# Kernel tuning notes

Measured on AMD Instinct MI355X. Metric: run time of the kernel, lower is better.

The kernel has to match this reference:

```python
import jax, jax.numpy as jnp
import numpy as np

N_MAP, N_ACT, B, E_PER, D = 131072, 1024, 16, 16384, 128
MAP_PER, ACT_PER = N_MAP // B, N_ACT // B
E = B * E_PER
EPS = 1e-5  # torch GroupNorm default eps


def _gn(x, g, b):
    # GroupNorm(1, C) on [N, C]: per-row normalization over channels
    m = jnp.mean(x, -1, keepdims=True)
    v = jnp.mean((x - m) ** 2, -1, keepdims=True)
    return (x - m) * jax.lax.rsqrt(v + EPS) * g + b


def _lin_gn(x, W, g, b, act=True):
    # LaneGCN Linear: nn.Linear(bias=False) -> GroupNorm(1, n_out) -> optional ReLU
    y = _gn(x @ W.T, g, b)
    return jax.nn.relu(y) if act else y


def setup_inputs() -> dict:
    key = jax.random.key(0)
    keys = iter(jax.random.split(key, 64))
    nrm = lambda shape, s=1.0: jax.random.normal(next(keys), shape, jnp.float32) * s
    uni = lambda shape, s=1.0: jax.random.uniform(next(keys), shape, jnp.float32) * s
    inp = {}
    inp['feat'] = nrm((N_MAP, D))
    inp['turn'] = nrm((N_MAP, 2))
    inp['control'] = uni((N_MAP,))
    inp['intersect'] = uni((N_MAP,))
    inp['map_ctrs'] = uni((N_MAP, 2), 100.0)
    inp['actors'] = nrm((N_ACT, D))
    inp['actor_ctrs'] = uni((N_ACT, 2), 100.0)
    # fixed within-scene edge list (stands in for the distance-threshold nonzero)
    rng = np.random.default_rng(0)
    hi = np.concatenate([rng.integers(b * MAP_PER, (b + 1) * MAP_PER, E_PER) for b in range(B)])
    wi = np.concatenate([rng.integers(b * ACT_PER, (b + 1) * ACT_PER, E_PER) for b in range(B)])
    inp['hi'] = jnp.asarray(hi, jnp.int32)
    inp['wi'] = jnp.asarray(wi, jnp.int32)
    # parameters
    W = lambda *s: nrm(s, 0.02)
    g_ = lambda *s: 1.0 + nrm(s, 0.05)
    b_ = lambda *s: nrm(s, 0.05)
    inp['meta_W'], inp['meta_g'], inp['meta_b'] = W(D, D + 4), g_(D), b_(D)
    inp['dW1'], inp['db1'] = W(2, D, 2), b_(2, D)
    inp['dW2'], inp['dg2'], inp['dbt2'] = W(2, D, D), g_(2, D), b_(2, D)
    inp['qW'], inp['qg'], inp['qb'] = W(2, D, D), g_(2, D), b_(2, D)
    inp['cW1'], inp['cg1'], inp['cb1'] = W(2, D, 3 * D), g_(2, D), b_(2, D)
    inp['cW2'] = W(2, D, D)
    inp['aW'] = W(2, D, D)
    inp['ng_g'], inp['ng_b'] = g_(2, D), b_(2, D)
    inp['lW'], inp['lg'], inp['lb'] = W(2, D, D), g_(2, D), b_(2, D)
    return inp


def reference(feat, turn, control, intersect, map_ctrs, actors, actor_ctrs, hi, wi,
              meta_W, meta_g, meta_b, dW1, db1, dW2, dg2, dbt2, qW, qg, qb,
              cW1, cg1, cb1, cW2, aW, ng_g, ng_b, lW, lg, lb):
    # meta fuse: concat(feat, turn, control, intersect) -> Linear+GN+ReLU
    meta = jnp.concatenate([feat, turn, control[:, None], intersect[:, None]], axis=1)
    feat = _lin_gn(meta, meta_W, meta_g, meta_b)
    for i in range(2):  # two Att blocks
        res = feat
        # dist branch: raw ctr offsets -> Linear(2,n_ctx)+ReLU -> Linear+GN+ReLU
        d = map_ctrs[hi] - actor_ctrs[wi]                       # [E, 2]
        d = jax.nn.relu(d @ dW1[i].T + db1[i])                  # [E, D]
        d = _lin_gn(d, dW2[i], dg2[i], dbt2[i])
        q = _lin_gn(feat[hi], qW[i], qg[i], qb[i])              # query on gathered agts
        c = jnp.concatenate([d, q, actors[wi]], axis=1)         # [E, 3D]
        c = _lin_gn(c, cW1[i], cg1[i], cb1[i])
        c = c @ cW2[i].T                                        # bias-free Linear
        a = feat @ aW[i].T                                      # self path, bias-free
        a = a.at[hi].add(c)                                     # scatter-add messages
        a = jax.nn.relu(_gn(a, ng_g[i], ng_b[i]))
        a = _lin_gn(a, lW[i], lg[i], lb[i], act=False)
        feat = jax.nn.relu(a + res)                             # use_relu=True
    return feat
```

## Files before the change

kernel.cpp:

```cpp
#include <hip/hip_runtime.h>
#include <stdint.h>

typedef unsigned short u16;
typedef __bf16 bf16x8 __attribute__((ext_vector_type(8)));
typedef float f32x4 __attribute__((ext_vector_type(4)));

#define MFMA(a, b, c) __builtin_amdgcn_mfma_f32_16x16x32_bf16(a, b, c, 0, 0, 0)

__device__ __forceinline__ u16 f2bf(float f) {
    union { float f; unsigned u; } v; v.f = f;
    unsigned r = v.u + 0x7fffu + ((v.u >> 16) & 1u);
    return (u16)(r >> 16);
}
__device__ __forceinline__ float bf2f(u16 h) {
    union { unsigned u; float f; } v; v.u = ((unsigned)h) << 16; return v.f;
}
__device__ __forceinline__ bf16x8 as_frag(uint4 u) {
    union { uint4 u; bf16x8 b; } v; v.u = u; return v.b;
}
__device__ __forceinline__ bf16x8 ldg_frag(const u16* p) {
    return as_frag(*reinterpret_cast<const uint4*>(p));
}
__device__ __forceinline__ int rowmap(int t, int i) {
    return 32 * (t >> 1) + 8 * (i >> 2) + 4 * (t & 1) + (i & 3);
}

template <int SRC_LDU>
__device__ __forceinline__ void stage128(const u16* __restrict__ src, u16* dst, int tid, int nt) {
    for (int c = tid; c < 2048; c += nt) {
        int row = c >> 4, j = c & 15;
        int js = (j & 8) | ((j ^ row) & 7);
        *reinterpret_cast<uint4*>(dst + row * 128 + js * 8) =
            *reinterpret_cast<const uint4*>(src + row * SRC_LDU + j * 8);
    }
}
__device__ __forceinline__ bf16x8 lds_w(const u16* base, int row, int byteoff) {
    int off = row * 256 + (byteoff ^ ((row & 7) << 4));
    return as_frag(*reinterpret_cast<const uint4*>(reinterpret_cast<const char*>(base) + off));
}

template <int KT>
__device__ __forceinline__ void gemm_acc(const bf16x8* a, const u16* __restrict__ W, int ldw,
                                         f32x4* acc, int c16, int q4) {
#pragma unroll
    for (int n = 0; n < 8; n++) {
        const u16* wp = W + (size_t)(n * 16 + c16) * ldw + q4 * 8;
#pragma unroll
        for (int k = 0; k < KT; k++) {
            bf16x8 b = ldg_frag(wp + k * 32);
            acc[n] = MFMA(a[k], b, acc[n]);
        }
    }
}

__device__ __forceinline__ void gn_t(f32x4* acc, const float* __restrict__ gb, bool relu, int q4) {
    float s = 0.f, s2 = 0.f;
#pragma unroll
    for (int t = 0; t < 8; t++)
#pragma unroll
        for (int r = 0; r < 4; r++) { float x = acc[t][r]; s += x; s2 = fmaf(x, x, s2); }
    s += __shfl_xor(s, 16, 64); s += __shfl_xor(s, 32, 64);
    s2 += __shfl_xor(s2, 16, 64); s2 += __shfl_xor(s2, 32, 64);
    float mean = s * (1.f / 128.f);
    float var = fmaf(s2, 1.f / 128.f, -mean * mean);
    float rstd = rsqrtf(var + 1e-5f);
#pragma unroll
    for (int t = 0; t < 8; t++) {
        const float4* g4 = reinterpret_cast<const float4*>(gb + (t * 16 + q4 * 4) * 2);
        float4 p01 = g4[0], p23 = g4[1];
        float gv[4] = {p01.x, p01.z, p23.x, p23.z};
        float bv[4] = {p01.y, p01.w, p23.y, p23.w};
#pragma unroll
        for (int r = 0; r < 4; r++) {
            float y = fmaf((acc[t][r] - mean) * rstd, gv[r], bv[r]);
            acc[t][r] = relu ? fmaxf(y, 0.f) : y;
        }
    }
}

__device__ __forceinline__ bf16x8 pack_frag(f32x4 lo, f32x4 hi) {
    union { u16 s[8]; bf16x8 b; } t;
#pragma unroll
    for (int j = 0; j < 4; j++) { t.s[j] = f2bf(lo[j]); t.s[4 + j] = f2bf(hi[j]); }
    return t.b;
}

__device__ __forceinline__ void gn_c(f32x4* acc, const float* __restrict__ g,
                                     const float* __restrict__ b, bool relu, int c16) {
    float gs[8], bs[8];
#pragma unroll
    for (int n = 0; n < 8; n++) { gs[n] = g[n * 16 + c16]; bs[n] = b[n * 16 + c16]; }
#pragma unroll
    for (int r = 0; r < 4; r++) {
        float s = 0.f, s2 = 0.f;
#pragma unroll
        for (int n = 0; n < 8; n++) { float x = acc[n][r]; s += x; s2 = fmaf(x, x, s2); }
#pragma unroll
        for (int m = 1; m < 16; m <<= 1) { s += __shfl_xor(s, m, 64); s2 += __shfl_xor(s2, m, 64); }
        float mean = s * (1.f / 128.f);
        float var = fmaf(s2, 1.f / 128.f, -mean * mean);
        float rstd = rsqrtf(var + 1e-5f);
#pragma unroll
        for (int n = 0; n < 8; n++) {
            float y = fmaf((acc[n][r] - mean) * rstd, gs[n], bs[n]);
            acc[n][r] = relu ? fmaxf(y, 0.f) : y;
        }
    }
}

__global__ __launch_bounds__(256) void k_prep(
    const float* __restrict__ dW2s, const float* __restrict__ qWs, const float* __restrict__ cW1s,
    const float* __restrict__ cW2s, const float* __restrict__ aWs, const float* __restrict__ lWs,
    const float* __restrict__ actors, const float* __restrict__ metaW,
    const float* __restrict__ dW1s, const float* __restrict__ db1s,
    const float* __restrict__ dg2s, const float* __restrict__ dbt2s,
    const float* __restrict__ qgs, const float* __restrict__ qbs,
    const float* __restrict__ cg1s, const float* __restrict__ cb1s,
    u16* __restrict__ o_dW2p, u16* __restrict__ o_qW, u16* __restrict__ o_cW1p,
    u16* __restrict__ o_cW2, u16* __restrict__ o_aW, u16* __restrict__ o_lW,
    u16* __restrict__ o_actb, u16* __restrict__ o_mWf, float* __restrict__ o_mWe,
    float* __restrict__ o_dw1p, float* __restrict__ o_gb) {
    int idx = blockIdx.x * 256 + threadIdx.x;
    if (idx >= 412672) return;
    if (idx < 32768) {
        int i = idx >> 14, rem = idx & 16383, ro = rem >> 7, col = rem & 127;
        o_dW2p[idx] = f2bf(dW2s[i * 16384 + rowmap(ro >> 4, ro & 15) * 128 + col]);
    } else if (idx < 65536) {
        int j = idx - 32768; o_qW[j] = f2bf(qWs[j]);
    } else if (idx < 163840) {
        int j = idx - 65536, i = j / 49152, rem = j - i * 49152, ro = rem / 384, col = rem - ro * 384;
        o_cW1p[j] = f2bf(cW1s[i * 49152 + rowmap(ro >> 4, ro & 15) * 384 + col]);
    } else if (idx < 196608) { int j = idx - 163840; o_cW2[j] = f2bf(cW2s[j]); }
    else if (idx < 229376) { int j = idx - 196608; o_aW[j] = f2bf(aWs[j]); }
    else if (idx < 262144) { int j = idx - 229376; o_lW[j] = f2bf(lWs[j]); }
    else if (idx < 393216) { int j = idx - 262144; o_actb[j] = f2bf(actors[j]); }
    else if (idx < 409600) { int j = idx - 393216; o_mWf[j] = f2bf(metaW[(j >> 7) * 132 + (j & 127)]); }
    else if (idx < 410112) { int j = idx - 409600; o_mWe[j] = metaW[(j >> 2) * 132 + 128 + (j & 3)]; }
    else if (idx < 411136) {
        int j = idx - 410112, i = j >> 9, col = (j >> 2) & 127, t = j & 3;
        float v = (t == 0) ? dW1s[i * 256 + col * 2]
                : (t == 1) ? dW1s[i * 256 + col * 2 + 1]
                : (t == 2) ? db1s[i * 128 + col] : 0.f;
        o_dw1p[j] = v;
    } else {
        int j = idx - 411136;
        int tb = j >> 9, rem = j & 511, i = rem >> 8, q = rem & 255, o = q >> 1, f = q & 1;
        const float* gsrc = (tb == 0) ? dg2s : (tb == 1) ? qgs : cg1s;
        const float* bsrc = (tb == 0) ? dbt2s : (tb == 1) ? qbs : cb1s;
        int src = i * 128 + rowmap(o >> 4, o & 15);
        o_gb[j] = f ? bsrc[src] : gsrc[src];
    }
}

__global__ __launch_bounds__(256) void k_meta(
    const float* __restrict__ feat, const float* __restrict__ turn,
    const float* __restrict__ ctrl, const float* __restrict__ inter,
    const u16* __restrict__ mWf, const float* __restrict__ mWe,
    const float* __restrict__ g, const float* __restrict__ b, u16* __restrict__ out) {
    int lane = threadIdx.x & 63, wv = threadIdx.x >> 6;
    int c16 = lane & 15, q4 = lane >> 4;
    int m0 = (blockIdx.x * 4 + wv) * 16;
    bf16x8 a[4];
    const float* xr = feat + (size_t)(m0 + c16) * 128 + q4 * 8;
#pragma unroll
    for (int k = 0; k < 4; k++) {
        float4 u0 = *reinterpret_cast<const float4*>(xr + k * 32);
        float4 u1 = *reinterpret_cast<const float4*>(xr + k * 32 + 4);
        union { u16 s[8]; bf16x8 b; } t;
        t.s[0] = f2bf(u0.x); t.s[1] = f2bf(u0.y); t.s[2] = f2bf(u0.z); t.s[3] = f2bf(u0.w);
        t.s[4] = f2bf(u1.x); t.s[5] = f2bf(u1.y); t.s[6] = f2bf(u1.z); t.s[7] = f2bf(u1.w);
        a[k] = t.b;
    }
    f32x4 acc[8] = {};
    gemm_acc<4>(a, mWf, 128, acc, c16, q4);
#pragma unroll
    for (int r = 0; r < 4; r++) {
        int row = m0 + q4 * 4 + r;
        float t0 = turn[2 * row], t1 = turn[2 * row + 1];
        float cv = ctrl[row], iv = inter[row];
#pragma unroll
        for (int n = 0; n < 8; n++) {
            int col = n * 16 + c16;
            float4 we = reinterpret_cast<const float4*>(mWe)[col];
            acc[n][r] += t0 * we.x + t1 * we.y + cv * we.z + iv * we.w;
        }
    }
    gn_c(acc, g, b, true, c16);
#pragma unroll
    for (int r = 0; r < 4; r++) {
        size_t row = m0 + q4 * 4 + r;
#pragma unroll
        for (int n = 0; n < 8; n++) out[row * 128 + n * 16 + c16] = f2bf(acc[n][r]);
    }
}

__global__ __launch_bounds__(256) void k_nodeA(
    const u16* __restrict__ featb, const u16* __restrict__ qW, const u16* __restrict__ aW,
    const float* __restrict__ qg, const float* __restrict__ qb,
    u16* __restrict__ q_out, float* __restrict__ a_out) {
    int lane = threadIdx.x & 63, wv = threadIdx.x >> 6;
    int c16 = lane & 15, q4 = lane >> 4;
    int m0 = (blockIdx.x * 4 + wv) * 16;
    bf16x8 a[4];
    const u16* xr = featb + (size_t)(m0 + c16) * 128 + q4 * 8;
#pragma unroll
    for (int k = 0; k < 4; k++) a[k] = ldg_frag(xr + k * 32);
    f32x4 accq[8] = {}, acca[8] = {};
    gemm_acc<4>(a, qW, 128, accq, c16, q4);
    gemm_acc<4>(a, aW, 128, acca, c16, q4);
#pragma unroll
    for (int r = 0; r < 4; r++) {
        size_t row = m0 + q4 * 4 + r;
#pragma unroll
        for (int n = 0; n < 8; n++) a_out[row * 128 + n * 16 + c16] = acca[n][r];
    }
    gn_c(accq, qg, qb, true, c16);
#pragma unroll
    for (int r = 0; r < 4; r++) {
        size_t row = m0 + q4 * 4 + r;
#pragma unroll
        for (int n = 0; n < 8; n++) q_out[row * 128 + n * 16 + c16] = f2bf(accq[n][r]);
    }
}

__global__ __launch_bounds__(256) void k_edge(
    const int* __restrict__ hi, const int* __restrict__ wi,
    const float* __restrict__ mctr, const float* __restrict__ actr,
    const float* __restrict__ dw1p, const u16* __restrict__ dW2p,
    const float* __restrict__ gb_d2,
    const u16* __restrict__ q_node, const u16* __restrict__ actb,
    const u16* __restrict__ cW1p, const float* __restrict__ gb_c1,
    const u16* __restrict__ cW2, float* __restrict__ a_out) {
    __shared__ u16 s0[16384];
    __shared__ u16 s1[16384];
    int tid = threadIdx.x;
    int lane = tid & 63, wv = tid >> 6;
    int c16 = lane & 15, q4 = lane >> 4;
    int bid = (int)blockIdx.x;
    bid = (bid & 7) * 256 + (bid >> 3);
    int ebase = bid * 128 + wv * 32;
    int h0 = hi[ebase + c16], w0 = wi[ebase + c16];
    int h1 = hi[ebase + 16 + c16], w1 = wi[ebase + 16 + c16];
    stage128<128>(dW2p, s0, tid, 256);
    stage128<384>(cW1p, s1, tid, 256);
    bf16x8 qf0[4], qf1[4], af0[4], af1[4];
    {
        const u16* qr0 = q_node + (size_t)h0 * 128 + q4 * 8;
        const u16* qr1 = q_node + (size_t)h1 * 128 + q4 * 8;
        const u16* ar0 = actb + (size_t)w0 * 128 + q4 * 8;
        const u16* ar1 = actb + (size_t)w1 * 128 + q4 * 8;
#pragma unroll
        for (int k = 0; k < 4; k++) {
            qf0[k] = ldg_frag(qr0 + k * 32); qf1[k] = ldg_frag(qr1 + k * 32);
            af0[k] = ldg_frag(ar0 + k * 32); af1[k] = ldg_frag(ar1 + k * 32);
        }
    }
    float dx0 = mctr[2 * h0] - actr[2 * w0], dy0 = mctr[2 * h0 + 1] - actr[2 * w0 + 1];
    float dx1 = mctr[2 * h1] - actr[2 * w1], dy1 = mctr[2 * h1 + 1] - actr[2 * w1 + 1];
    bf16x8 bd0[4], bd1[4];
    const float4* w4p = reinterpret_cast<const float4*>(dw1p);
#pragma unroll
    for (int k = 0; k < 4; k++) {
        union { u16 s[8]; uint4 u; } t0, t1;
#pragma unroll
        for (int j = 0; j < 8; j++) {
            float4 w4 = w4p[k * 32 + q4 * 8 + j];
            t0.s[j] = f2bf(fmaxf(fmaf(dx0, w4.x, fmaf(dy0, w4.y, w4.z)), 0.f));
            t1.s[j] = f2bf(fmaxf(fmaf(dx1, w4.x, fmaf(dy1, w4.y, w4.z)), 0.f));
        }
        bd0[k] = as_frag(t0.u); bd1[k] = as_frag(t1.u);
    }
    __syncthreads();
    f32x4 accA[8] = {}, accB[8] = {};
#pragma unroll
    for (int k = 0; k < 4; k++)
#pragma unroll
        for (int t = 0; t < 8; t++) {
            bf16x8 a = lds_w(s0, t * 16 + c16, k * 64 + q4 * 16);
            accA[t] = MFMA(a, bd0[k], accA[t]);
            accB[t] = MFMA(a, bd1[k], accB[t]);
        }
    gn_t(accA, gb_d2, true, q4);
    gn_t(accB, gb_d2, true, q4);
    bf16x8 d2f0[4], d2f1[4];
#pragma unroll
    for (int k = 0; k < 4; k++) {
        d2f0[k] = pack_frag(accA[2 * k], accA[2 * k + 1]);
        d2f1[k] = pack_frag(accB[2 * k], accB[2 * k + 1]);
    }
    f32x4 cA[8] = {}, cB[8] = {};
#pragma unroll
    for (int k = 0; k < 4; k++)
#pragma unroll
        for (int t = 0; t < 8; t++) {
            bf16x8 a = lds_w(s1, t * 16 + c16, k * 64 + q4 * 16);
            cA[t] = MFMA(a, d2f0[k], cA[t]);
            cB[t] = MFMA(a, d2f1[k], cB[t]);
        }
    __syncthreads();
    stage128<384>(cW1p + 128, s0, tid, 256);
    stage128<384>(cW1p + 256, s1, tid, 256);
    __syncthreads();
#pragma unroll
    for (int k = 0; k < 4; k++)
#pragma unroll
        for (int t = 0; t < 8; t++) {
            bf16x8 a = lds_w(s0, t * 16 + c16, k * 64 + q4 * 16);
            cA[t] = MFMA(a, qf0[k], cA[t]);
            cB[t] = MFMA(a, qf1[k], cB[t]);
        }
#pragma unroll
    for (int k = 0; k < 4; k++)
#pragma unroll
        for (int t = 0; t < 8; t++) {
            bf16x8 a = lds_w(s1, t * 16 + c16, k * 64 + q4 * 16);
            cA[t] = MFMA(a, af0[k], cA[t]);
            cB[t] = MFMA(a, af1[k], cB[t]);
        }
    __syncthreads();
    stage128<128>(cW2, s0, tid, 256);
    gn_t(cA, gb_c1, true, q4);
    gn_t(cB, gb_c1, true, q4);
    bf16x8 ba0[4], ba1[4];
#pragma unroll
    for (int k = 0; k < 4; k++) {
        ba0[k] = pack_frag(cA[2 * k], cA[2 * k + 1]);
        ba1[k] = pack_frag(cB[2 * k], cB[2 * k + 1]);
    }
    __syncthreads();
    f32x4 oA[8] = {}, oB[8] = {};
#pragma unroll
    for (int k = 0; k < 4; k++)
#pragma unroll
        for (int n = 0; n < 8; n++) {
            bf16x8 b = lds_w(s0, n * 16 + c16, k * 64 + q4 * 16);
            oA[n] = MFMA(ba0[k], b, oA[n]);
            oB[n] = MFMA(ba1[k], b, oB[n]);
        }
#pragma unroll
    for (int r = 0; r < 4; r++) {
        int hr0 = hi[ebase + q4 * 4 + r];
        int hr1 = hi[ebase + 16 + q4 * 4 + r];
        float* dst0 = a_out + (size_t)hr0 * 128 + c16;
        float* dst1 = a_out + (size_t)hr1 * 128 + c16;
#pragma unroll
        for (int n = 0; n < 8; n++) {
            unsafeAtomicAdd(dst0 + n * 16, oA[n][r]);
            unsafeAtomicAdd(dst1 + n * 16, oB[n][r]);
        }
    }
}

__global__ __launch_bounds__(256) void k_nodeB(
    const float* __restrict__ a_in, const float* __restrict__ gg, const float* __restrict__ gb,
    const u16* __restrict__ lW, const float* __restrict__ lg, const float* __restrict__ lb,
    const u16* __restrict__ res, u16* __restrict__ out_bf, float* __restrict__ out_f32) {
    int lane = threadIdx.x & 63, wv = threadIdx.x >> 6;
    int c16 = lane & 15, q4 = lane >> 4;
    int m0 = (blockIdx.x * 4 + wv) * 16;
    const float* xr = a_in + (size_t)(m0 + c16) * 128 + q4 * 8;
    float x[32];
#pragma unroll
    for (int k = 0; k < 4; k++) {
        float4 u0 = *reinterpret_cast<const float4*>(xr + k * 32);
        float4 u1 = *reinterpret_cast<const float4*>(xr + k * 32 + 4);
        x[k * 8 + 0] = u0.x; x[k * 8 + 1] = u0.y; x[k * 8 + 2] = u0.z; x[k * 8 + 3] = u0.w;
        x[k * 8 + 4] = u1.x; x[k * 8 + 5] = u1.y; x[k * 8 + 6] = u1.z; x[k * 8 + 7] = u1.w;
    }
    float s = 0.f, s2 = 0.f;
#pragma unroll
    for (int t = 0; t < 32; t++) { s += x[t]; s2 = fmaf(x[t], x[t], s2); }
    s += __shfl_xor(s, 16, 64); s += __shfl_xor(s, 32, 64);
    s2 += __shfl_xor(s2, 16, 64); s2 += __shfl_xor(s2, 32, 64);
    float mean = s * (1.f / 128.f);
    float var = fmaf(s2, 1.f / 128.f, -mean * mean);
    float rstd = rsqrtf(var + 1e-5f);
    bf16x8 a[4];
#pragma unroll
    for (int k = 0; k < 4; k++) {
        float4 g0 = *reinterpret_cast<const float4*>(gg + k * 32 + q4 * 8);
        float4 g1 = *reinterpret_cast<const float4*>(gg + k * 32 + q4 * 8 + 4);
        float4 b0 = *reinterpret_cast<const float4*>(gb + k * 32 + q4 * 8);
        float4 b1 = *reinterpret_cast<const float4*>(gb + k * 32 + q4 * 8 + 4);
        float gv[8] = {g0.x, g0.y, g0.z, g0.w, g1.x, g1.y, g1.z, g1.w};
        float bv[8] = {b0.x, b0.y, b0.z, b0.w, b1.x, b1.y, b1.z, b1.w};
        union { u16 s[8]; bf16x8 b; } t;
#pragma unroll
        for (int j = 0; j < 8; j++) {
            float y = fmaf((x[k * 8 + j] - mean) * rstd, gv[j], bv[j]);
            t.s[j] = f2bf(fmaxf(y, 0.f));
        }
        a[k] = t.b;
    }
    f32x4 acc[8] = {};
    gemm_acc<4>(a, lW, 128, acc, c16, q4);
    gn_c(acc, lg, lb, false, c16);
#pragma unroll
    for (int r = 0; r < 4; r++) {
        size_t row = m0 + q4 * 4 + r;
#pragma unroll
        for (int n = 0; n < 8; n++) {
            int col = n * 16 + c16;
            float y = acc[n][r] + bf2f(res[row * 128 + col]);
            y = fmaxf(y, 0.f);
            if (out_bf) out_bf[row * 128 + col] = f2bf(y);
            else out_f32[row * 128 + col] = y;
        }
    }
}

extern "C" void kernel_launch(void* const* d_in, const int* in_sizes, int n_in,
                              void* d_out, int out_size, void* d_ws, size_t ws_size,
                              hipStream_t stream) {
    const float* feat = (const float*)d_in[0];
    const float* turn = (const float*)d_in[1];
    const float* ctrl = (const float*)d_in[2];
    const float* inter = (const float*)d_in[3];
    const float* mctr = (const float*)d_in[4];
    const float* actors = (const float*)d_in[5];
    const float* actr = (const float*)d_in[6];
    const int* hi = (const int*)d_in[7];
    const int* wi = (const int*)d_in[8];
    const float* metaW = (const float*)d_in[9];
    const float* metag = (const float*)d_in[10];
    const float* metab = (const float*)d_in[11];
    const float* dW1 = (const float*)d_in[12];
    const float* db1 = (const float*)d_in[13];
    const float* dW2 = (const float*)d_in[14];
    const float* dg2 = (const float*)d_in[15];
    const float* dbt2 = (const float*)d_in[16];
    const float* qW = (const float*)d_in[17];
    const float* qg = (const float*)d_in[18];
    const float* qb = (const float*)d_in[19];
    const float* cW1 = (const float*)d_in[20];
    const float* cg1 = (const float*)d_in[21];
    const float* cb1 = (const float*)d_in[22];
    const float* cW2 = (const float*)d_in[23];
    const float* aW = (const float*)d_in[24];
    const float* ngg = (const float*)d_in[25];
    const float* ngb = (const float*)d_in[26];
    const float* lW = (const float*)d_in[27];
    const float* lg = (const float*)d_in[28];
    const float* lb = (const float*)d_in[29];

    char* ws = (char*)d_ws;
    u16* feat0 = (u16*)(ws);
    u16* feat1 = (u16*)(ws + 33554432);
    u16* qbuf = (u16*)(ws + 67108864);
    u16* actb = (u16*)(ws + 100663296);
    u16* wmWf = (u16*)(ws + 100925440);
    u16* wdW2p = (u16*)(ws + 100958208);
    u16* wqW = (u16*)(ws + 101023744);
    u16* wcW1p = (u16*)(ws + 101089280);
    u16* wcW2 = (u16*)(ws + 101285888);
    u16* waW = (u16*)(ws + 101351424);
    u16* wlW = (u16*)(ws + 101416960);
    float* wmWe = (float*)(ws + 101482496);
    float* wdw1p = (float*)(ws + 101484544);
    float* gball = (float*)(ws + 101488640);
    float* abuf = (float*)d_out;

    k_prep<<<1613, 256, 0, stream>>>(dW2, qW, cW1, cW2, aW, lW, actors, metaW, dW1, db1,
                                     dg2, dbt2, qg, qb, cg1, cb1,
                                     wdW2p, wqW, wcW1p, wcW2, waW, wlW, actb, wmWf, wmWe,
                                     wdw1p, gball);
    k_meta<<<2048, 256, 0, stream>>>(feat, turn, ctrl, inter, wmWf, wmWe, metag, metab, feat0);
    for (int i = 0; i < 2; i++) {
        const u16* fcur = i ? feat1 : feat0;
        k_nodeA<<<2048, 256, 0, stream>>>(fcur, wqW + i * 16384, waW + i * 16384,
                                          qg + i * 128, qb + i * 128, qbuf, abuf);
        k_edge<<<2048, 256, 0, stream>>>(hi, wi, mctr, actr, wdw1p + i * 512, wdW2p + i * 16384,
                                         gball + i * 256, qbuf, actb,
                                         wcW1p + i * 49152, gball + 1024 + i * 256,
                                         wcW2 + i * 16384, abuf);
        k_nodeB<<<2048, 256, 0, stream>>>(abuf, ngg + i * 128, ngb + i * 128, wlW + i * 16384,
                                          lg + i * 128, lb + i * 128, fcur,
                                          i ? nullptr : feat1, i ? (float*)d_out : nullptr);
    }
}
```

Baseline: 672.1 us.

## Precompute q and actor projections of cW1 per node instead of per edge

Splits the cW1 linear over the concatenated [d, q, actor] input into three 128x128 pieces. The q and actor pieces are applied once per map node (in k_nodeA) and once per actor (new k_act kernel), rather than once per edge. The edge kernel now gathers these precomputed partial products and adds them before GroupNorm, which removes two thirds of the per-edge cW1 MFMA work and the LDS staging for it. The cost is one extra GEMM per node, a small extra kernel, and bf16 rounding of the partial sums before accumulation.

```diff
diff --git a/kernel.cpp b/kernel.cpp
--- a/kernel.cpp
+++ b/kernel.cpp
@@ -111,39 +111,46 @@
 __global__ __launch_bounds__(256) void k_prep(
     const float* __restrict__ dW2s, const float* __restrict__ qWs, const float* __restrict__ cW1s,
     const float* __restrict__ cW2s, const float* __restrict__ aWs, const float* __restrict__ lWs,
-    const float* __restrict__ actors, const float* __restrict__ metaW,
+    const float* __restrict__ metaW,
     const float* __restrict__ dW1s, const float* __restrict__ db1s,
     const float* __restrict__ dg2s, const float* __restrict__ dbt2s,
     const float* __restrict__ qgs, const float* __restrict__ qbs,
     const float* __restrict__ cg1s, const float* __restrict__ cb1s,
-    u16* __restrict__ o_dW2p, u16* __restrict__ o_qW, u16* __restrict__ o_cW1p,
+    u16* __restrict__ o_dW2p, u16* __restrict__ o_qWp, u16* __restrict__ o_cW10,
+    u16* __restrict__ o_cW1q, u16* __restrict__ o_cW1a,
     u16* __restrict__ o_cW2, u16* __restrict__ o_aW, u16* __restrict__ o_lW,
-    u16* __restrict__ o_actb, u16* __restrict__ o_mWf, float* __restrict__ o_mWe,
+    u16* __restrict__ o_mWf, float* __restrict__ o_mWe,
     float* __restrict__ o_dw1p, float* __restrict__ o_gb) {
     int idx = blockIdx.x * 256 + threadIdx.x;
-    if (idx >= 412672) return;
+    if (idx >= 281600) return;
     if (idx < 32768) {
         int i = idx >> 14, rem = idx & 16383, ro = rem >> 7, col = rem & 127;
         o_dW2p[idx] = f2bf(dW2s[i * 16384 + rowmap(ro >> 4, ro & 15) * 128 + col]);
     } else if (idx < 65536) {
-        int j = idx - 32768; o_qW[j] = f2bf(qWs[j]);
+        int j = idx - 32768, i = j >> 14, rem = j & 16383, ro = rem >> 7, col = rem & 127;
+        o_qWp[j] = f2bf(qWs[i * 16384 + rowmap(ro >> 4, ro & 15) * 128 + col]);
+    } else if (idx < 98304) {
+        int j = idx - 65536, i = j >> 14, rem = j & 16383, ro = rem >> 7, col = rem & 127;
+        o_cW10[j] = f2bf(cW1s[i * 49152 + rowmap(ro >> 4, ro & 15) * 384 + col]);
+    } else if (idx < 131072) {
+        int j = idx - 98304, i = j >> 14, rem = j & 16383, ro = rem >> 7, col = rem & 127;
+        o_cW1q[j] = f2bf(cW1s[i * 49152 + rowmap(ro >> 4, ro & 15) * 384 + 128 + col]);
     } else if (idx < 163840) {
-        int j = idx - 65536, i = j / 49152, rem = j - i * 49152, ro = rem / 384, col = rem - ro * 384;
-        o_cW1p[j] = f2bf(cW1s[i * 49152 + rowmap(ro >> 4, ro & 15) * 384 + col]);
+        int j = idx - 131072, i = j >> 14, rem = j & 16383, ro = rem >> 7, col = rem & 127;
+        o_cW1a[j] = f2bf(cW1s[i * 49152 + rowmap(ro >> 4, ro & 15) * 384 + 256 + col]);
     } else if (idx < 196608) { int j = idx - 163840; o_cW2[j] = f2bf(cW2s[j]); }
     else if (idx < 229376) { int j = idx - 196608; o_aW[j] = f2bf(aWs[j]); }
     else if (idx < 262144) { int j = idx - 229376; o_lW[j] = f2bf(lWs[j]); }
-    else if (idx < 393216) { int j = idx - 262144; o_actb[j] = f2bf(actors[j]); }
-    else if (idx < 409600) { int j = idx - 393216; o_mWf[j] = f2bf(metaW[(j >> 7) * 132 + (j & 127)]); }
-    else if (idx < 410112) { int j = idx - 409600; o_mWe[j] = metaW[(j >> 2) * 132 + 128 + (j & 3)]; }
-    else if (idx < 411136) {
-        int j = idx - 410112, i = j >> 9, col = (j >> 2) & 127, t = j & 3;
+    else if (idx < 278528) { int j = idx - 262144; o_mWf[j] = f2bf(metaW[(j >> 7) * 132 + (j & 127)]); }
+    else if (idx < 279040) { int j = idx - 278528; o_mWe[j] = metaW[(j >> 2) * 132 + 128 + (j & 3)]; }
+    else if (idx < 280064) {
+        int j = idx - 279040, i = j >> 9, col = (j >> 2) & 127, t = j & 3;
         float v = (t == 0) ? dW1s[i * 256 + col * 2]
                 : (t == 1) ? dW1s[i * 256 + col * 2 + 1]
                 : (t == 2) ? db1s[i * 128 + col] : 0.f;
         o_dw1p[j] = v;
     } else {
-        int j = idx - 411136;
+        int j = idx - 280064;
         int tb = j >> 9, rem = j & 511, i = rem >> 8, q = rem & 255, o = q >> 1, f = q & 1;
         const float* gsrc = (tb == 0) ? dg2s : (tb == 1) ? qgs : cg1s;
         const float* bsrc = (tb == 0) ? dbt2s : (tb == 1) ? qbs : cb1s;
@@ -194,32 +201,85 @@
     }
 }
 
+__global__ __launch_bounds__(256) void k_act(
+    const float* __restrict__ actors, const u16* __restrict__ cW1ap, u16* __restrict__ ac_out) {
+    int lane = threadIdx.x & 63, wv = threadIdx.x >> 6;
+    int c16 = lane & 15, q4 = lane >> 4;
+    int b = (int)blockIdx.x;
+    int i = b >> 4;
+    int row = ((b & 15) * 4 + wv) * 16 + c16;
+    const float* xr = actors + (size_t)row * 128 + q4 * 8;
+    bf16x8 f[4];
+#pragma unroll
+    for (int k = 0; k < 4; k++) {
+        union { u16 s[8]; uint4 u; } t;
+#pragma unroll
+        for (int j = 0; j < 8; j++) t.s[j] = f2bf(xr[k * 32 + j]);
+        f[k] = as_frag(t.u);
+    }
+    const u16* Wp = cW1ap + i * 16384;
+    f32x4 acc[8] = {};
+#pragma unroll
+    for (int k = 0; k < 4; k++)
+#pragma unroll
+        for (int t = 0; t < 8; t++) {
+            bf16x8 a = ldg_frag(Wp + (size_t)(t * 16 + c16) * 128 + k * 32 + q4 * 8);
+            acc[t] = MFMA(a, f[k], acc[t]);
+        }
+    u16* dst = ac_out + (size_t)i * 131072 + (size_t)row * 128 + q4 * 8;
+#pragma unroll
+    for (int T = 0; T < 4; T++) {
+        bf16x8 p = pack_frag(acc[2 * T], acc[2 * T + 1]);
+        union { bf16x8 b; uint4 u; } v; v.b = p;
+        *reinterpret_cast<uint4*>(dst + T * 32) = v.u;
+    }
+}
+
 __global__ __launch_bounds__(256) void k_nodeA(
-    const u16* __restrict__ featb, const u16* __restrict__ qW, const u16* __restrict__ aW,
-    const float* __restrict__ qg, const float* __restrict__ qb,
-    u16* __restrict__ q_out, float* __restrict__ a_out) {
+    const u16* __restrict__ featb, const u16* __restrict__ qWp, const u16* __restrict__ aW,
+    const float* __restrict__ gb_q, const u16* __restrict__ cW1qp,
+    u16* __restrict__ qc_out, float* __restrict__ a_out) {
     int lane = threadIdx.x & 63, wv = threadIdx.x >> 6;
     int c16 = lane & 15, q4 = lane >> 4;
     int m0 = (blockIdx.x * 4 + wv) * 16;
-    bf16x8 a[4];
+    bf16x8 f[4];
     const u16* xr = featb + (size_t)(m0 + c16) * 128 + q4 * 8;
 #pragma unroll
-    for (int k = 0; k < 4; k++) a[k] = ldg_frag(xr + k * 32);
-    f32x4 accq[8] = {}, acca[8] = {};
-    gemm_acc<4>(a, qW, 128, accq, c16, q4);
-    gemm_acc<4>(a, aW, 128, acca, c16, q4);
+    for (int k = 0; k < 4; k++) f[k] = ldg_frag(xr + k * 32);
+    f32x4 acca[8] = {};
+    gemm_acc<4>(f, aW, 128, acca, c16, q4);
 #pragma unroll
     for (int r = 0; r < 4; r++) {
         size_t row = m0 + q4 * 4 + r;
 #pragma unroll
         for (int n = 0; n < 8; n++) a_out[row * 128 + n * 16 + c16] = acca[n][r];
     }
-    gn_c(accq, qg, qb, true, c16);
-#pragma unroll
-    for (int r = 0; r < 4; r++) {
-        size_t row = m0 + q4 * 4 + r;
-#pragma unroll
-        for (int n = 0; n < 8; n++) q_out[row * 128 + n * 16 + c16] = f2bf(accq[n][r]);
+    f32x4 accq[8] = {};
+#pragma unroll
+    for (int k = 0; k < 4; k++)
+#pragma unroll
+        for (int t = 0; t < 8; t++) {
+            bf16x8 a = ldg_frag(qWp + (size_t)(t * 16 + c16) * 128 + k * 32 + q4 * 8);
+            accq[t] = MFMA(a, f[k], accq[t]);
+        }
+    gn_t(accq, gb_q, true, q4);
+    bf16x8 qf[4];
+#pragma unroll
+    for (int k = 0; k < 4; k++) qf[k] = pack_frag(accq[2 * k], accq[2 * k + 1]);
+    f32x4 acc2[8] = {};
+#pragma unroll
+    for (int k = 0; k < 4; k++)
+#pragma unroll
+        for (int t = 0; t < 8; t++) {
+            bf16x8 a = ldg_frag(cW1qp + (size_t)(t * 16 + c16) * 128 + k * 32 + q4 * 8);
+            acc2[t] = MFMA(a, qf[k], acc2[t]);
+        }
+    u16* dst = qc_out + (size_t)(m0 + c16) * 128 + q4 * 8;
+#pragma unroll
+    for (int T = 0; T < 4; T++) {
+        bf16x8 p = pack_frag(acc2[2 * T], acc2[2 * T + 1]);
+        union { bf16x8 b; uint4 u; } v; v.b = p;
+        *reinterpret_cast<uint4*>(dst + T * 32) = v.u;
     }
 }
 
@@ -228,8 +288,8 @@
     const float* __restrict__ mctr, const float* __restrict__ actr,
     const float* __restrict__ dw1p, const u16* __restrict__ dW2p,
     const float* __restrict__ gb_d2,
-    const u16* __restrict__ q_node, const u16* __restrict__ actb,
-    const u16* __restrict__ cW1p, const float* __restrict__ gb_c1,
+    const u16* __restrict__ qc, const u16* __restrict__ ac,
+    const u16* __restrict__ cW10p, const float* __restrict__ gb_c1,
     const u16* __restrict__ cW2, float* __restrict__ a_out) {
     __shared__ u16 s0[16384];
     __shared__ u16 s1[16384];
@@ -242,18 +302,15 @@
     int h0 = hi[ebase + c16], w0 = wi[ebase + c16];
     int h1 = hi[ebase + 16 + c16], w1 = wi[ebase + 16 + c16];
     stage128<128>(dW2p, s0, tid, 256);
-    stage128<384>(cW1p, s1, tid, 256);
-    bf16x8 qf0[4], qf1[4], af0[4], af1[4];
-    {
-        const u16* qr0 = q_node + (size_t)h0 * 128 + q4 * 8;
-        const u16* qr1 = q_node + (size_t)h1 * 128 + q4 * 8;
-        const u16* ar0 = actb + (size_t)w0 * 128 + q4 * 8;
-        const u16* ar1 = actb + (size_t)w1 * 128 + q4 * 8;
-#pragma unroll
-        for (int k = 0; k < 4; k++) {
-            qf0[k] = ldg_frag(qr0 + k * 32); qf1[k] = ldg_frag(qr1 + k * 32);
-            af0[k] = ldg_frag(ar0 + k * 32); af1[k] = ldg_frag(ar1 + k * 32);
-        }
+    stage128<128>(cW10p, s1, tid, 256);
+    union F8 { bf16x8 b; uint4 u; u16 s[8]; };
+    F8 qg0[4], qg1[4], ag0[4], ag1[4];
+#pragma unroll
+    for (int T = 0; T < 4; T++) {
+        qg0[T].b = ldg_frag(qc + (size_t)h0 * 128 + T * 32 + q4 * 8);
+        qg1[T].b = ldg_frag(qc + (size_t)h1 * 128 + T * 32 + q4 * 8);
+        ag0[T].b = ldg_frag(ac + (size_t)w0 * 128 + T * 32 + q4 * 8);
+        ag1[T].b = ldg_frag(ac + (size_t)w1 * 128 + T * 32 + q4 * 8);
     }
     float dx0 = mctr[2 * h0] - actr[2 * w0], dy0 = mctr[2 * h0 + 1] - actr[2 * w0 + 1];
     float dx1 = mctr[2 * h1] - actr[2 * w1], dy1 = mctr[2 * h1 + 1] - actr[2 * w1 + 1];
@@ -288,6 +345,8 @@
         d2f0[k] = pack_frag(accA[2 * k], accA[2 * k + 1]);
         d2f1[k] = pack_frag(accB[2 * k], accB[2 * k + 1]);
     }
+    __syncthreads();
+    stage128<128>(cW2, s0, tid, 256);
     f32x4 cA[8] = {}, cB[8] = {};
 #pragma unroll
     for (int k = 0; k < 4; k++)
@@ -297,28 +356,15 @@
             cA[t] = MFMA(a, d2f0[k], cA[t]);
             cB[t] = MFMA(a, d2f1[k], cB[t]);
         }
-    __syncthreads();
-    stage128<384>(cW1p + 128, s0, tid, 256);
-    stage128<384>(cW1p + 256, s1, tid, 256);
-    __syncthreads();
-#pragma unroll
-    for (int k = 0; k < 4; k++)
-#pragma unroll
-        for (int t = 0; t < 8; t++) {
-            bf16x8 a = lds_w(s0, t * 16 + c16, k * 64 + q4 * 16);
-            cA[t] = MFMA(a, qf0[k], cA[t]);
-            cB[t] = MFMA(a, qf1[k], cB[t]);
-        }
-#pragma unroll
-    for (int k = 0; k < 4; k++)
-#pragma unroll
-        for (int t = 0; t < 8; t++) {
-            bf16x8 a = lds_w(s1, t * 16 + c16, k * 64 + q4 * 16);
-            cA[t] = MFMA(a, af0[k], cA[t]);
-            cB[t] = MFMA(a, af1[k], cB[t]);
-        }
-    __syncthreads();
-    stage128<128>(cW2, s0, tid, 256);
+#pragma unroll
+    for (int t = 0; t < 8; t++) {
+        int T = t >> 1, base = 4 * (t & 1);
+#pragma unroll
+        for (int r = 0; r < 4; r++) {
+            cA[t][r] += bf2f(qg0[T].s[base + r]) + bf2f(ag0[T].s[base + r]);
+            cB[t][r] += bf2f(qg1[T].s[base + r]) + bf2f(ag1[T].s[base + r]);
+        }
+    }
     gn_t(cA, gb_c1, true, q4);
     gn_t(cB, gb_c1, true, q4);
     bf16x8 ba0[4], ba1[4];
@@ -446,32 +492,36 @@
     char* ws = (char*)d_ws;
     u16* feat0 = (u16*)(ws);
     u16* feat1 = (u16*)(ws + 33554432);
-    u16* qbuf = (u16*)(ws + 67108864);
-    u16* actb = (u16*)(ws + 100663296);
-    u16* wmWf = (u16*)(ws + 100925440);
-    u16* wdW2p = (u16*)(ws + 100958208);
-    u16* wqW = (u16*)(ws + 101023744);
-    u16* wcW1p = (u16*)(ws + 101089280);
-    u16* wcW2 = (u16*)(ws + 101285888);
-    u16* waW = (u16*)(ws + 101351424);
-    u16* wlW = (u16*)(ws + 101416960);
-    float* wmWe = (float*)(ws + 101482496);
-    float* wdw1p = (float*)(ws + 101484544);
-    float* gball = (float*)(ws + 101488640);
+    u16* qcbuf = (u16*)(ws + 67108864);
+    u16* acbuf = (u16*)(ws + 100663296);
+    u16* wdW2p = (u16*)(ws + 101187584);
+    u16* wqWp = (u16*)(ws + 101253120);
+    u16* wcW10 = (u16*)(ws + 101318656);
+    u16* wcW1q = (u16*)(ws + 101384192);
+    u16* wcW1a = (u16*)(ws + 101449728);
+    u16* wcW2 = (u16*)(ws + 101515264);
+    u16* waW = (u16*)(ws + 101580800);
+    u16* wlW = (u16*)(ws + 101646336);
+    u16* wmWf = (u16*)(ws + 101711872);
+    float* wmWe = (float*)(ws + 101744640);
+    float* wdw1p = (float*)(ws + 101746688);
+    float* gball = (float*)(ws + 101750784);
     float* abuf = (float*)d_out;
 
-    k_prep<<<1613, 256, 0, stream>>>(dW2, qW, cW1, cW2, aW, lW, actors, metaW, dW1, db1,
+    k_prep<<<1100, 256, 0, stream>>>(dW2, qW, cW1, cW2, aW, lW, metaW, dW1, db1,
                                      dg2, dbt2, qg, qb, cg1, cb1,
-                                     wdW2p, wqW, wcW1p, wcW2, waW, wlW, actb, wmWf, wmWe,
-                                     wdw1p, gball);
+                                     wdW2p, wqWp, wcW10, wcW1q, wcW1a, wcW2, waW, wlW,
+                                     wmWf, wmWe, wdw1p, gball);
     k_meta<<<2048, 256, 0, stream>>>(feat, turn, ctrl, inter, wmWf, wmWe, metag, metab, feat0);
+    k_act<<<32, 256, 0, stream>>>(actors, wcW1a, acbuf);
     for (int i = 0; i < 2; i++) {
         const u16* fcur = i ? feat1 : feat0;
-        k_nodeA<<<2048, 256, 0, stream>>>(fcur, wqW + i * 16384, waW + i * 16384,
-                                          qg + i * 128, qb + i * 128, qbuf, abuf);
+        k_nodeA<<<2048, 256, 0, stream>>>(fcur, wqWp + i * 16384, waW + i * 16384,
+                                          gball + 512 + i * 256, wcW1q + i * 16384,
+                                          qcbuf, abuf);
         k_edge<<<2048, 256, 0, stream>>>(hi, wi, mctr, actr, wdw1p + i * 512, wdW2p + i * 16384,
-                                         gball + i * 256, qbuf, actb,
-                                         wcW1p + i * 49152, gball + 1024 + i * 256,
+                                         gball + i * 256, qcbuf, acbuf + i * 131072,
+                                         wcW10 + i * 16384, gball + 1024 + i * 256,
                                          wcW2 + i * 16384, abuf);
         k_nodeB<<<2048, 256, 0, stream>>>(abuf, ngg + i * 128, ngb + i * 128, wlW + i * 16384,
                                           lg + i * 128, lb + i * 128, fcur,
```

New measurement: 697.3 us (median of 2 runs). 1.04x slower.
